# Kernel optimization log

Measured on AMD Instinct MI355X. Metric: run time of the kernel, lower is better.

The kernel has to match this reference:

```python
import jax, jax.numpy as jnp
import numpy as np

EPS = 1e-7


def squash(s):
    # safe norm over last axis, keepdims
    norm = jnp.sqrt(jnp.sum(jnp.square(s), axis=-1, keepdims=True) + EPS)
    norm_sq = jnp.square(norm)
    return norm_sq / (1.0 + norm_sq) / norm * s


def setup_inputs() -> dict:
    key = jax.random.key(0)
    k1, k2 = jax.random.split(key)
    B, IN_CAPS, IN_DIM = 64, 2048, 16
    N_CAPS, CAP_DIM = 64, 16
    x = jax.random.normal(k1, (B, IN_CAPS, IN_DIM), dtype=jnp.float32)
    # glorot-uniform-ish init for W
    limit = (6.0 / (IN_DIM + N_CAPS * CAP_DIM)) ** 0.5
    W = jax.random.uniform(k2, (IN_CAPS, IN_DIM, N_CAPS * CAP_DIM),
                           minval=-limit, maxval=limit, dtype=jnp.float32)
    bias = jnp.zeros((N_CAPS, CAP_DIM), dtype=jnp.float32)
    return {"x": x, "W": W, "bias": bias}


def reference(x, W, bias):
    B, in_caps, in_dim = x.shape
    n_caps, cap_dim = bias.shape
    r_iters = 3
    # projection: [B, in_caps, n_caps*cap_dim] -> [B, in_caps, n_caps, cap_dim]
    u_hat = jnp.einsum('bij,ijk->bik', x, W).reshape(B, in_caps, n_caps, cap_dim)
    b = jnp.zeros((B, in_caps, n_caps, 1), dtype=u_hat.dtype)
    v = None
    for r in range(r_iters):
        c = jax.nn.softmax(b, axis=2)                       # route over class caps
        s = jnp.sum(u_hat * c, axis=1, keepdims=True)       # [B, 1, n_caps, cap_dim]
        s = s + bias
        v = squash(s)
        if r < r_iters - 1:
            agreement = jnp.sum(u_hat * v, axis=-1, keepdims=True)
            b = b + agreement
    return jnp.squeeze(v, axis=1)                           # [B, n_caps, cap_dim]
```

## Files before the change

kernel.cpp:

```cpp
#include <hip/hip_runtime.h>
#include <hip/hip_bf16.h>
#include <hip/hip_fp16.h>
#include <cstdio>

#define B_  64
#define I_  2048
#define J_  16
#define N_  64
#define D_  16
#define K_  1024

using short8 = __attribute__((ext_vector_type(8))) short;
using f32x4  = __attribute__((ext_vector_type(4))) float;

#if __has_builtin(__builtin_amdgcn_cvt_pk_u8_f32)
#define CVTPK_U8(f, sel, old) (unsigned)__builtin_amdgcn_cvt_pk_u8_f32((f), (sel), (old))
#else
__device__ __forceinline__ unsigned cvtpk_u8_sw(float f, unsigned sel, unsigned old) {
  unsigned b = (unsigned)(int)f & 0xffu;
  unsigned sh = sel * 8u;
  return (old & ~(0xffu << sh)) | (b << sh);
}
#define CVTPK_U8(f, sel, old) cvtpk_u8_sw((f), (sel), (old))
#endif

__device__ __forceinline__ short8 pack_bf16x8(float a0, float a1, float a2, float a3,
                                              float a4, float a5, float a6, float a7) {
  __hip_bfloat162 p0 = __float22bfloat162_rn(float2{a0, a1});
  __hip_bfloat162 p1 = __float22bfloat162_rn(float2{a2, a3});
  __hip_bfloat162 p2 = __float22bfloat162_rn(float2{a4, a5});
  __hip_bfloat162 p3 = __float22bfloat162_rn(float2{a6, a7});
  union { unsigned u[4]; short8 s; } cv;
  cv.u[0] = *(unsigned*)&p0; cv.u[1] = *(unsigned*)&p1;
  cv.u[2] = *(unsigned*)&p2; cv.u[3] = *(unsigned*)&p3;
  return cv.s;
}

__global__ __launch_bounds__(256) void project_k(const float* __restrict__ x,
                                                 const float* __restrict__ W,
                                                 unsigned char* __restrict__ uh,
                                                 unsigned short* __restrict__ sc) {
  const int i  = blockIdx.x;
  const int t  = threadIdx.x;
  const int l  = t & 63;
  const int wv = t >> 6;

  __shared__ unsigned short lds_w[256 * 20];
  __shared__ float          lds_x[64 * 20];
  __shared__ unsigned int   out_lds[64 * 64];
  __shared__ unsigned short sc_lds[64 * 20];

  {
    int b = t >> 2, q = t & 3;
    float4 v = ((const float4*)(x + ((size_t)b * I_ + i) * J_))[q];
    *(float4*)&lds_x[b * 20 + q * 4] = v;
  }
  __syncthreads();

  short8 xfrag = {0, 0, 0, 0, 0, 0, 0, 0};
  if (l < 32) {
    int b = wv * 16 + (l & 15);
    const float* xp = &lds_x[b * 20 + (l >> 4) * 8];
    float4 f0 = *(const float4*)xp;
    float4 f1 = *(const float4*)(xp + 4);
    xfrag = pack_bf16x8(f0.x, f0.y, f0.z, f0.w, f1.x, f1.y, f1.z, f1.w);
  }

  for (int ph = 0; ph < 4; ++ph) {
    {
      const float* wp = W + (size_t)i * (J_ * K_) + ph * 256 + t;
      float wj[J_];
#pragma unroll
      for (int j = 0; j < J_; ++j) wj[j] = wp[(size_t)j * K_];
#pragma unroll
      for (int q = 0; q < 4; ++q) {
        __hip_bfloat162 pA = __float22bfloat162_rn(float2{wj[4*q+0], wj[4*q+1]});
        __hip_bfloat162 pB = __float22bfloat162_rn(float2{wj[4*q+2], wj[4*q+3]});
        uint2 u; u.x = *(unsigned*)&pA; u.y = *(unsigned*)&pB;
        *(uint2*)&lds_w[t * 20 + q * 4] = u;
      }
    }
    __syncthreads();

#pragma unroll
    for (int ntl = 0; ntl < 16; ++ntl) {
      short8 afrag = {0, 0, 0, 0, 0, 0, 0, 0};
      if (l < 32) {
        int krow = ntl * 16 + (l & 15);
        const unsigned short* ap = &lds_w[krow * 20 + (l >> 4) * 8];
        union { uint2 u2[2]; short8 s; } cv;
        cv.u2[0] = *(const uint2*)ap;
        cv.u2[1] = *(const uint2*)(ap + 4);
        afrag = cv.s;
      }
      f32x4 acc = {0.f, 0.f, 0.f, 0.f};
      acc = __builtin_amdgcn_mfma_f32_16x16x32_bf16(afrag, xfrag, acc, 0, 0, 0);

      const int b = wv * 16 + (l & 15);
      float ax = fmaxf(fmaxf(fabsf(acc[0]), fabsf(acc[1])),
                       fmaxf(fabsf(acc[2]), fabsf(acc[3])));
      ax = fmaxf(ax, __shfl_xor(ax, 16));
      ax = fmaxf(ax, __shfl_xor(ax, 32));
      float inv = __fdividef(127.0f, fmaxf(ax, 1e-30f));
      float e0 = rintf(fmaf(acc[0], inv, 128.f));
      float e1 = rintf(fmaf(acc[1], inv, 128.f));
      float e2 = rintf(fmaf(acc[2], inv, 128.f));
      float e3 = rintf(fmaf(acc[3], inv, 128.f));
      unsigned pk = CVTPK_U8(e0, 0u, 0u);
      pk = CVTPK_U8(e1, 1u, pk);
      pk = CVTPK_U8(e2, 2u, pk);
      pk = CVTPK_U8(e3, 3u, pk);
      int kd = ntl * 4 + (l >> 4);
      out_lds[b * 64 + (kd ^ ((b & 7) << 2))] = pk;
      if (l < 16)
        sc_lds[b * 20 + ntl] = __half_as_ushort(__float2half_rn(ax * (1.0f / 127.0f)));
    }
    __syncthreads();

    {
      int c = t & 15;
#pragma unroll
      for (int it = 0; it < 4; ++it) {
        int b = (t >> 4) + it * 16;
        uint4 v = *(const uint4*)&out_lds[b * 64 + ((c * 4) ^ ((b & 7) << 2))];
        *(uint4*)(uh + (size_t)b * I_ * K_ + (size_t)i * K_ + ph * 256 + c * 16) = v;
      }
      int b2 = t >> 2, n4 = (t & 3) * 4;
      uint2 sv = *(const uint2*)&sc_lds[b2 * 20 + n4];
      *(uint2*)(sc + (size_t)b2 * I_ * N_ + (size_t)i * N_ + ph * 16 + n4) = sv;
    }
    __syncthreads();
  }
}

template <int MODE>
__global__ __launch_bounds__(256, 4) void route_k(const unsigned char* __restrict__ uh,
                                                  const unsigned short* __restrict__ sc,
                                                  const float* __restrict__ sa,
                                                  const float* __restrict__ sb,
                                                  const float* __restrict__ bias,
                                                  float* __restrict__ s_out) {
  const int t    = threadIdx.x;
  const int lane = t & 63;
  const int wv   = t >> 6;
  const int b    = blockIdx.x >> 4;
  const int iw   = ((blockIdx.x & 15) << 2) + wv;
  const int i0   = iw * 32;

  float vsum[16];
  float voff = 0.f;
  if (MODE >= 1) {
    float bs[16];
#pragma unroll
    for (int q = 0; q < 4; ++q) {
      float4 bb4 = *(const float4*)&bias[lane * 16 + q * 4];
      bs[q*4+0] = bb4.x; bs[q*4+1] = bb4.y; bs[q*4+2] = bb4.z; bs[q*4+3] = bb4.w;
    }
    {
      float va[16], nn = 0.f;
#pragma unroll
      for (int q = 0; q < 4; ++q) {
        float4 tmp = *(const float4*)&sa[(size_t)b * K_ + lane * 16 + q * 4];
        va[q*4+0] = tmp.x + bs[q*4+0]; va[q*4+1] = tmp.y + bs[q*4+1];
        va[q*4+2] = tmp.z + bs[q*4+2]; va[q*4+3] = tmp.w + bs[q*4+3];
      }
#pragma unroll
      for (int d = 0; d < 16; ++d) nn += va[d] * va[d];
      float n2 = nn + 1e-7f;
      float f = sqrtf(n2) / (1.0f + n2);
#pragma unroll
      for (int d = 0; d < 16; ++d) vsum[d] = va[d] * f;
    }
    if (MODE == 2) {
      float vb[16], nn = 0.f;
#pragma unroll
      for (int q = 0; q < 4; ++q) {
        float4 tmp = *(const float4*)&sb[(size_t)b * K_ + lane * 16 + q * 4];
        vb[q*4+0] = tmp.x + bs[q*4+0]; vb[q*4+1] = tmp.y + bs[q*4+1];
        vb[q*4+2] = tmp.z + bs[q*4+2]; vb[q*4+3] = tmp.w + bs[q*4+3];
      }
#pragma unroll
      for (int d = 0; d < 16; ++d) nn += vb[d] * vb[d];
      float n2 = nn + 1e-7f;
      float f = sqrtf(n2) / (1.0f + n2);
#pragma unroll
      for (int d = 0; d < 16; ++d) vsum[d] += vb[d] * f;
    }
    float tv = 0.f;
#pragma unroll
    for (int d = 0; d < 16; ++d) tv += vsum[d];
    voff = 128.0f * tv;
  }

  constexpr int IPW = 32;
  constexpr int PF  = 4;

  const unsigned char*  base = uh + (size_t)b * I_ * K_ + lane * 16;
  const unsigned short* scb  = sc + (size_t)b * I_ * N_ + lane;

  uint4 dbuf[PF];
  unsigned short hbuf[PF];
#pragma unroll
  for (int p = 0; p < PF; ++p) {
    int ip = (i0 + p) & (I_ - 1);
    dbuf[p] = *(const uint4*)(base + (size_t)ip * K_);
    hbuf[p] = scb[(size_t)ip * N_];
  }

  float s_loc[16];
#pragma unroll
  for (int d = 0; d < 16; ++d) s_loc[d] = 0.f;
  float csum = 0.f;

  for (int ii = 0; ii < IPW; ii += PF) {
#pragma unroll
    for (int p = 0; p < PF; ++p) {
      float scale = __half2float(__ushort_as_half(hbuf[p]));
      float u[16];
      {
        unsigned wd;
        wd = dbuf[p].x;
        u[0]  = (float)(wd & 0xffu);         u[1]  = (float)((wd >> 8) & 0xffu);
        u[2]  = (float)((wd >> 16) & 0xffu); u[3]  = (float)(wd >> 24);
        wd = dbuf[p].y;
        u[4]  = (float)(wd & 0xffu);         u[5]  = (float)((wd >> 8) & 0xffu);
        u[6]  = (float)((wd >> 16) & 0xffu); u[7]  = (float)(wd >> 24);
        wd = dbuf[p].z;
        u[8]  = (float)(wd & 0xffu);         u[9]  = (float)((wd >> 8) & 0xffu);
        u[10] = (float)((wd >> 16) & 0xffu); u[11] = (float)(wd >> 24);
        wd = dbuf[p].w;
        u[12] = (float)(wd & 0xffu);         u[13] = (float)((wd >> 8) & 0xffu);
        u[14] = (float)((wd >> 16) & 0xffu); u[15] = (float)(wd >> 24);
      }

      int ip = (i0 + ii + p + PF) & (I_ - 1);
      dbuf[p] = *(const uint4*)(base + (size_t)ip * K_);
      hbuf[p] = scb[(size_t)ip * N_];

      if (MODE == 0) {
#pragma unroll
        for (int d = 0; d < 16; ++d) s_loc[d] = fmaf(scale, u[d], s_loc[d]);
        csum += scale;
      } else {
        float dot = 0.f;
#pragma unroll
        for (int d = 0; d < 16; ++d) dot = fmaf(u[d], vsum[d], dot);
        float bl = scale * (dot - voff);
        float m = bl;
        m = fmaxf(m, __shfl_xor(m, 1));
        m = fmaxf(m, __shfl_xor(m, 2));
        m = fmaxf(m, __shfl_xor(m, 4));
        m = fmaxf(m, __shfl_xor(m, 8));
        m = fmaxf(m, __shfl_xor(m, 16));
        m = fmaxf(m, __shfl_xor(m, 32));
        float e = __expf(bl - m);
        float ss = e;
        ss += __shfl_xor(ss, 1);
        ss += __shfl_xor(ss, 2);
        ss += __shfl_xor(ss, 4);
        ss += __shfl_xor(ss, 8);
        ss += __shfl_xor(ss, 16);
        ss += __shfl_xor(ss, 32);
        float cs = __fdividef(e, ss) * scale;
#pragma unroll
        for (int d = 0; d < 16; ++d) s_loc[d] = fmaf(cs, u[d], s_loc[d]);
        csum += cs;
      }
    }
  }

#pragma unroll
  for (int d = 0; d < 16; ++d) s_loc[d] -= 128.0f * csum;
  if (MODE == 0) {
#pragma unroll
    for (int d = 0; d < 16; ++d) s_loc[d] *= (1.0f / 64.0f);
  }

  __shared__ float sred[4][64 * 17];
#pragma unroll
  for (int d = 0; d < 16; ++d) sred[wv][lane * 17 + d] = s_loc[d];
  __syncthreads();
#pragma unroll
  for (int e = 0; e < 4; ++e) {
    int idx = t * 4 + e;
    int n = idx >> 4, d = idx & 15;
    float val = sred[0][n*17+d] + sred[1][n*17+d] + sred[2][n*17+d] + sred[3][n*17+d];
    atomicAdd(&s_out[(size_t)b * K_ + idx], val);
  }
}

__global__ __launch_bounds__(256) void squash_k(const float* __restrict__ s_in,
                                                const float* __restrict__ bias,
                                                float* __restrict__ v_out) {
  const int b = blockIdx.x, t = threadIdx.x, k0 = t * 4;
  float4 s = *(const float4*)&s_in[b * K_ + k0];
  float4 bb = *(const float4*)&bias[k0];
  s.x += bb.x; s.y += bb.y; s.z += bb.z; s.w += bb.w;
  float p = s.x * s.x + s.y * s.y + s.z * s.z + s.w * s.w;
  p += __shfl_xor(p, 1);
  p += __shfl_xor(p, 2);
  float n2 = p + 1e-7f;
  float nrm = sqrtf(n2);
  float f = nrm / (1.0f + n2);
  float4 o = {s.x * f, s.y * f, s.z * f, s.w * f};
  *(float4*)&v_out[b * K_ + k0] = o;
}

extern "C" void kernel_launch(void* const* d_in, const int* in_sizes, int n_in,
                              void* d_out, int out_size, void* d_ws, size_t ws_size,
                              hipStream_t stream) {
  const float* x    = (const float*)d_in[0];
  const float* W    = (const float*)d_in[1];
  const float* bias = (const float*)d_in[2];
  float* out = (float*)d_out;

  char* ws = (char*)d_ws;
  size_t off = 0;
  unsigned char*  uh = (unsigned char*)(ws + off);  off += (size_t)B_ * I_ * K_;
  unsigned short* sc = (unsigned short*)(ws + off); off += (size_t)B_ * I_ * N_ * 2;
  float* s0 = (float*)(ws + off); off += (size_t)B_ * K_ * 4;
  float* s1 = (float*)(ws + off); off += (size_t)B_ * K_ * 4;
  float* s2 = (float*)(ws + off); off += (size_t)B_ * K_ * 4;

  if (ws_size < off)
    fprintf(stderr, "ClassCapsule: ws_size=%zu < needed=%zu — expect corruption\n", ws_size, off);

  (void)hipMemsetAsync(s0, 0, (size_t)3 * B_ * K_ * 4, stream);

  project_k<<<dim3(I_), dim3(256), 0, stream>>>(x, W, uh, sc);

  route_k<0><<<dim3(1024), dim3(256), 0, stream>>>(uh, sc, nullptr, nullptr, bias, s0);
  route_k<1><<<dim3(1024), dim3(256), 0, stream>>>(uh, sc, s0, nullptr, bias, s1);
  route_k<2><<<dim3(1024), dim3(256), 0, stream>>>(uh, sc, s0, s1, bias, s2);
  squash_k<<<dim3(B_), dim3(256), 0, stream>>>(s2, bias, out);
}
```

Measured before the change: 171.6 us.

## Use 32x32x16 bf16 MFMA for projection and vectorize W loads

New measurement: 166.8 us. 2.8% less time.

```diff
diff --git a/kernel.cpp b/kernel.cpp
--- a/kernel.cpp
+++ b/kernel.cpp
@@ -11,7 +11,7 @@
 #define K_  1024
 
 using short8 = __attribute__((ext_vector_type(8))) short;
-using f32x4  = __attribute__((ext_vector_type(4))) float;
+using f32x16 = __attribute__((ext_vector_type(16))) float;
 
 #if __has_builtin(__builtin_amdgcn_cvt_pk_u8_f32)
 #define CVTPK_U8(f, sel, old) (unsigned)__builtin_amdgcn_cvt_pk_u8_f32((f), (sel), (old))
@@ -44,6 +44,8 @@
   const int t  = threadIdx.x;
   const int l  = t & 63;
   const int wv = t >> 6;
+  const int h  = l >> 5;
+  const int lr = l & 31;
 
   __shared__ unsigned short lds_w[256 * 20];
   __shared__ float          lds_x[64 * 20];
@@ -57,73 +59,93 @@
   }
   __syncthreads();
 
-  short8 xfrag = {0, 0, 0, 0, 0, 0, 0, 0};
-  if (l < 32) {
-    int b = wv * 16 + (l & 15);
-    const float* xp = &lds_x[b * 20 + (l >> 4) * 8];
+  short8 xfrag;
+  {
+    int b = (wv & 1) * 32 + lr;
+    const float* xp = &lds_x[b * 20 + h * 8];
     float4 f0 = *(const float4*)xp;
     float4 f1 = *(const float4*)(xp + 4);
     xfrag = pack_bf16x8(f0.x, f0.y, f0.z, f0.w, f1.x, f1.y, f1.z, f1.w);
   }
 
+  const int b  = (wv & 1) * 32 + lr;
+  const unsigned sw = (unsigned)((b & 7) << 2);
+  const int kt_base = (wv >> 1) * 4;
+
   for (int ph = 0; ph < 4; ++ph) {
     {
-      const float* wp = W + (size_t)i * (J_ * K_) + ph * 256 + t;
-      float wj[J_];
-#pragma unroll
-      for (int j = 0; j < J_; ++j) wj[j] = wp[(size_t)j * K_];
-#pragma unroll
-      for (int q = 0; q < 4; ++q) {
-        __hip_bfloat162 pA = __float22bfloat162_rn(float2{wj[4*q+0], wj[4*q+1]});
-        __hip_bfloat162 pB = __float22bfloat162_rn(float2{wj[4*q+2], wj[4*q+3]});
+      const float* wp = W + (size_t)i * (J_ * K_) + ph * 256;
+      const int j0 = (t & 3) * 4;
+      const int kg = t >> 2;
+      float4 r0 = *(const float4*)(wp + (size_t)(j0 + 0) * K_ + kg * 4);
+      float4 r1 = *(const float4*)(wp + (size_t)(j0 + 1) * K_ + kg * 4);
+      float4 r2 = *(const float4*)(wp + (size_t)(j0 + 2) * K_ + kg * 4);
+      float4 r3 = *(const float4*)(wp + (size_t)(j0 + 3) * K_ + kg * 4);
+      const float* p0 = (const float*)&r0;
+      const float* p1 = (const float*)&r1;
+      const float* p2 = (const float*)&r2;
+      const float* p3 = (const float*)&r3;
+#pragma unroll
+      for (int kk = 0; kk < 4; ++kk) {
+        __hip_bfloat162 pA = __float22bfloat162_rn(float2{p0[kk], p1[kk]});
+        __hip_bfloat162 pB = __float22bfloat162_rn(float2{p2[kk], p3[kk]});
         uint2 u; u.x = *(unsigned*)&pA; u.y = *(unsigned*)&pB;
-        *(uint2*)&lds_w[t * 20 + q * 4] = u;
+        *(uint2*)&lds_w[(kg * 4 + kk) * 20 + j0] = u;
       }
     }
     __syncthreads();
 
 #pragma unroll
-    for (int ntl = 0; ntl < 16; ++ntl) {
-      short8 afrag = {0, 0, 0, 0, 0, 0, 0, 0};
-      if (l < 32) {
-        int krow = ntl * 16 + (l & 15);
-        const unsigned short* ap = &lds_w[krow * 20 + (l >> 4) * 8];
-        union { uint2 u2[2]; short8 s; } cv;
-        cv.u2[0] = *(const uint2*)ap;
-        cv.u2[1] = *(const uint2*)(ap + 4);
-        afrag = cv.s;
-      }
-      f32x4 acc = {0.f, 0.f, 0.f, 0.f};
-      acc = __builtin_amdgcn_mfma_f32_16x16x32_bf16(afrag, xfrag, acc, 0, 0, 0);
-
-      const int b = wv * 16 + (l & 15);
-      float ax = fmaxf(fmaxf(fabsf(acc[0]), fabsf(acc[1])),
-                       fmaxf(fabsf(acc[2]), fabsf(acc[3])));
-      ax = fmaxf(ax, __shfl_xor(ax, 16));
-      ax = fmaxf(ax, __shfl_xor(ax, 32));
-      float inv = __fdividef(127.0f, fmaxf(ax, 1e-30f));
-      float e0 = rintf(fmaf(acc[0], inv, 128.f));
-      float e1 = rintf(fmaf(acc[1], inv, 128.f));
-      float e2 = rintf(fmaf(acc[2], inv, 128.f));
-      float e3 = rintf(fmaf(acc[3], inv, 128.f));
-      unsigned pk = CVTPK_U8(e0, 0u, 0u);
-      pk = CVTPK_U8(e1, 1u, pk);
-      pk = CVTPK_U8(e2, 2u, pk);
-      pk = CVTPK_U8(e3, 3u, pk);
-      int kd = ntl * 4 + (l >> 4);
-      out_lds[b * 64 + (kd ^ ((b & 7) << 2))] = pk;
-      if (l < 16)
-        sc_lds[b * 20 + ntl] = __half_as_ushort(__float2half_rn(ax * (1.0f / 127.0f)));
+    for (int kk = 0; kk < 4; ++kk) {
+      const int kt = kt_base + kk;
+      const unsigned short* ap = &lds_w[(kt * 32 + lr) * 20 + h * 8];
+      union { uint2 u2[2]; short8 s; } cv;
+      cv.u2[0] = *(const uint2*)ap;
+      cv.u2[1] = *(const uint2*)(ap + 4);
+      f32x16 acc = {0.f, 0.f, 0.f, 0.f, 0.f, 0.f, 0.f, 0.f,
+                    0.f, 0.f, 0.f, 0.f, 0.f, 0.f, 0.f, 0.f};
+      acc = __builtin_amdgcn_mfma_f32_32x32x16_bf16(cv.s, xfrag, acc, 0, 0, 0);
+
+#define QCAP(C8, CS) do {                                                       \
+      float ax = fabsf(acc[(C8) + 0]);                                          \
+      ax = fmaxf(ax, fabsf(acc[(C8) + 1]));                                     \
+      ax = fmaxf(ax, fabsf(acc[(C8) + 2]));                                     \
+      ax = fmaxf(ax, fabsf(acc[(C8) + 3]));                                     \
+      ax = fmaxf(ax, fabsf(acc[(C8) + 4]));                                     \
+      ax = fmaxf(ax, fabsf(acc[(C8) + 5]));                                     \
+      ax = fmaxf(ax, fabsf(acc[(C8) + 6]));                                     \
+      ax = fmaxf(ax, fabsf(acc[(C8) + 7]));                                     \
+      ax = fmaxf(ax, __shfl_xor(ax, 32));                                       \
+      float inv = __fdividef(127.0f, fmaxf(ax, 1e-30f));                        \
+      unsigned pk0 = CVTPK_U8(rintf(fmaf(acc[(C8) + 0], inv, 128.f)), 0u, 0u);  \
+      pk0 = CVTPK_U8(rintf(fmaf(acc[(C8) + 1], inv, 128.f)), 1u, pk0);          \
+      pk0 = CVTPK_U8(rintf(fmaf(acc[(C8) + 2], inv, 128.f)), 2u, pk0);          \
+      pk0 = CVTPK_U8(rintf(fmaf(acc[(C8) + 3], inv, 128.f)), 3u, pk0);          \
+      unsigned pk1 = CVTPK_U8(rintf(fmaf(acc[(C8) + 4], inv, 128.f)), 0u, 0u);  \
+      pk1 = CVTPK_U8(rintf(fmaf(acc[(C8) + 5], inv, 128.f)), 1u, pk1);          \
+      pk1 = CVTPK_U8(rintf(fmaf(acc[(C8) + 6], inv, 128.f)), 2u, pk1);          \
+      pk1 = CVTPK_U8(rintf(fmaf(acc[(C8) + 7], inv, 128.f)), 3u, pk1);          \
+      const int ibase = kt * 8 + (CS) * 4;                                      \
+      out_lds[b * 64 + ((unsigned)(ibase + h)     ^ sw)] = pk0;                 \
+      out_lds[b * 64 + ((unsigned)(ibase + 2 + h) ^ sw)] = pk1;                 \
+      if (h == 0)                                                               \
+        sc_lds[b * 20 + kt * 2 + (CS)] =                                        \
+            __half_as_ushort(__float2half_rn(ax * (1.0f / 127.0f)));            \
+    } while (0)
+
+      QCAP(0, 0);
+      QCAP(8, 1);
+#undef QCAP
     }
     __syncthreads();
 
     {
-      int c = t & 15;
+      const int c = t & 15;
 #pragma unroll
       for (int it = 0; it < 4; ++it) {
-        int b = (t >> 4) + it * 16;
-        uint4 v = *(const uint4*)&out_lds[b * 64 + ((c * 4) ^ ((b & 7) << 2))];
-        *(uint4*)(uh + (size_t)b * I_ * K_ + (size_t)i * K_ + ph * 256 + c * 16) = v;
+        int bf = (t >> 4) + it * 16;
+        uint4 v = *(const uint4*)&out_lds[bf * 64 + (((unsigned)(c * 4)) ^ ((unsigned)((bf & 7) << 2)))];
+        *(uint4*)(uh + (size_t)bf * I_ * K_ + (size_t)i * K_ + ph * 256 + c * 16) = v;
       }
       int b2 = t >> 2, n4 = (t & 3) * 4;
       uint2 sv = *(const uint2*)&sc_lds[b2 * 20 + n4];
```
